# Performance work log

Measured on AMD Instinct MI355X. Metric: run time of the kernel, lower is better.

Reference implementation:

```python
import jax, jax.numpy as jnp
import numpy as np

LR = 0.01
EPS = 1e-8
D, H, O, N = 1024, 256, 64, 1024


def _normalize(W, b):
    # L2 (Frobenius) normalize weights and biases, clamped at EPS
    wn = jnp.maximum(jnp.sqrt(jnp.sum(W * W)), EPS)
    bn = jnp.maximum(jnp.sqrt(jnp.sum(b * b)), EPS)
    return W / wn, b / bn


def _step(carry, xt):
    W1, b1, W2, b2, W3, b3 = carry
    x, t = xt
    # forward pass (3-layer sigmoid MLP, softmax over -a3 as in original)
    a1 = jax.nn.sigmoid(x @ W1 + b1)
    a2 = jax.nn.sigmoid(a1 @ W2 + b2)
    a3 = jax.nn.sigmoid(a2 @ W3 + b3)
    out = jax.nn.softmax(-a3)
    # manual backprop deltas
    d3 = (t - out) * a3 * (1.0 - a3)
    o2 = (W3 @ d3) * a2 * (1.0 - a2)
    o1 = (W2 @ o2) * a1 * (1.0 - a1)
    # SGD update (note: original subtracts the delta, matching .sub_)
    W3 = W3 - LR * jnp.outer(a2, d3)
    b3 = b3 - LR * d3
    W2 = W2 - LR * jnp.outer(a1, o2)
    b2 = b2 - LR * o2
    W1 = W1 - LR * jnp.outer(x, o1)
    b1 = b1 - LR * o1
    # L2 normalize each layer's weights/biases
    W1, b1 = _normalize(W1, b1)
    W2, b2 = _normalize(W2, b2)
    W3, b3 = _normalize(W3, b3)
    return (W1, b1, W2, b2, W3, b3), None


def setup_inputs() -> dict:
    key = jax.random.key(0)
    k = jax.random.split(key, 5)
    return {
        "training_data": jax.random.normal(k[0], (N, D), jnp.float32),
        "training_targets": jax.random.uniform(k[1], (N, O), dtype=jnp.float32),
        "weights1": jax.random.normal(k[2], (D, H), jnp.float32) * 0.01,
        "biases1": jnp.zeros((H,), jnp.float32),
        "weights2": jax.random.normal(k[3], (H, H), jnp.float32) * 0.01,
        "biases2": jnp.zeros((H,), jnp.float32),
        "weights3": jax.random.normal(k[4], (H, O), jnp.float32) * 0.01,
        "biases3": jnp.zeros((O,), jnp.float32),
    }


def reference(training_data, training_targets, weights1, biases1, weights2, biases2, weights3, biases3):
    carry0 = (weights1, biases1, weights2, biases2, weights3, biases3)
    carry, _ = jax.lax.scan(_step, carry0, (training_data, training_targets))
    W1, b1, W2, b2, W3, b3 = carry
    return (W1, W2, W3)
```

## Files before the change

### kernel.cpp

```cpp
#include <hip/hip_runtime.h>
#include <math.h>


#define LRC  0.01f
#define EPSV 1e-8f

typedef float f32x8 __attribute__((ext_vector_type(8)));

#define SMEM_FLOATS 36368
#define SMEM_BYTES  (SMEM_FLOATS * 4)

#define ROWS16(OP)                                                            \
  OP(0) OP(1) OP(2) OP(3) OP(4) OP(5) OP(6) OP(7)                             \
  OP(8) OP(9) OP(10) OP(11) OP(12) OP(13) OP(14) OP(15)

__device__ __forceinline__ float hsum8(f32x8 v) {
  return ((v.s0 + v.s1) + (v.s2 + v.s3)) + ((v.s4 + v.s5) + (v.s6 + v.s7));
}

__device__ __forceinline__ float wave_allred(float v) {
#pragma unroll
  for (int off = 32; off > 0; off >>= 1) v += __shfl_xor(v, off);
  return v;
}

#define FMA16(c, a, b)                                                        \
  c[0][0] += a.x * b.x; c[0][1] += a.x * b.y; c[0][2] += a.x * b.z; c[0][3] += a.x * b.w; \
  c[1][0] += a.y * b.x; c[1][1] += a.y * b.y; c[1][2] += a.y * b.z; c[1][3] += a.y * b.w; \
  c[2][0] += a.z * b.x; c[2][1] += a.z * b.y; c[2][2] += a.z * b.z; c[2][3] += a.z * b.w; \
  c[3][0] += a.w * b.x; c[3][1] += a.w * b.y; c[3][2] += a.w * b.z; c[3][3] += a.w * b.w;

__global__ __launch_bounds__(256) void k_gram(const float* __restrict__ X,
                                              float* __restrict__ G) {
  const int bi = blockIdx.y, bj = blockIdx.x;
  if (bj > bi) return;
  __shared__ float Xa[32][68];
  __shared__ float Xb[32][68];
  const int tid = threadIdx.x;
  const int tx = tid & 15, ty = tid >> 4;
  float c[4][4] = {};
  for (int k0 = 0; k0 < 1024; k0 += 32) {
    __syncthreads();
    {
      const int row = tid >> 2, kk = (tid & 3) * 8;
      const float* pa = X + (bi * 64 + row) * 1024 + k0 + kk;
      const float4 a0 = *(const float4*)pa;
      const float4 a1 = *(const float4*)(pa + 4);
      Xa[kk + 0][row] = a0.x; Xa[kk + 1][row] = a0.y;
      Xa[kk + 2][row] = a0.z; Xa[kk + 3][row] = a0.w;
      Xa[kk + 4][row] = a1.x; Xa[kk + 5][row] = a1.y;
      Xa[kk + 6][row] = a1.z; Xa[kk + 7][row] = a1.w;
      const float* pb = X + (bj * 64 + row) * 1024 + k0 + kk;
      const float4 b0 = *(const float4*)pb;
      const float4 b1 = *(const float4*)(pb + 4);
      Xb[kk + 0][row] = b0.x; Xb[kk + 1][row] = b0.y;
      Xb[kk + 2][row] = b0.z; Xb[kk + 3][row] = b0.w;
      Xb[kk + 4][row] = b1.x; Xb[kk + 5][row] = b1.y;
      Xb[kk + 6][row] = b1.z; Xb[kk + 7][row] = b1.w;
    }
    __syncthreads();
#pragma unroll
    for (int kk = 0; kk < 32; kk++) {
      const float4 a = *(const float4*)&Xa[kk][ty * 4];
      const float4 b = *(const float4*)&Xb[kk][tx * 4];
      FMA16(c, a, b)
    }
  }
#pragma unroll
  for (int ii = 0; ii < 4; ii++) {
    *(float4*)(G + (bi * 64 + ty * 4 + ii) * 1024 + bj * 64 + tx * 4) =
        make_float4(c[ii][0], c[ii][1], c[ii][2], c[ii][3]);
  }
}

__global__ __launch_bounds__(256) void k_z10(const float* __restrict__ X,
                                             const float* __restrict__ W1g,
                                             float* __restrict__ Z10) {
  const int bi = blockIdx.y, bj = blockIdx.x;
  __shared__ float At[32][68];
  __shared__ float Bt[32][68];
  const int tid = threadIdx.x;
  const int tx = tid & 15, ty = tid >> 4;
  float c[4][4] = {};
  for (int k0 = 0; k0 < 1024; k0 += 32) {
    __syncthreads();
    {
      const int row = tid >> 2, kk = (tid & 3) * 8;
      const float* pa = X + (bi * 64 + row) * 1024 + k0 + kk;
      const float4 a0 = *(const float4*)pa;
      const float4 a1 = *(const float4*)(pa + 4);
      At[kk + 0][row] = a0.x; At[kk + 1][row] = a0.y;
      At[kk + 2][row] = a0.z; At[kk + 3][row] = a0.w;
      At[kk + 4][row] = a1.x; At[kk + 5][row] = a1.y;
      At[kk + 6][row] = a1.z; At[kk + 7][row] = a1.w;
      const int kr = tid >> 3, j8 = (tid & 7) * 8;
      const float* pb = W1g + (k0 + kr) * 256 + bj * 64 + j8;
      *(float4*)&Bt[kr][j8]     = *(const float4*)pb;
      *(float4*)&Bt[kr][j8 + 4] = *(const float4*)(pb + 4);
    }
    __syncthreads();
#pragma unroll
    for (int kk = 0; kk < 32; kk++) {
      const float4 a = *(const float4*)&At[kk][ty * 4];
      const float4 b = *(const float4*)&Bt[kk][tx * 4];
      FMA16(c, a, b)
    }
  }
#pragma unroll
  for (int ii = 0; ii < 4; ii++) {
    *(float4*)(Z10 + (bi * 64 + ty * 4 + ii) * 256 + bj * 64 + tx * 4) =
        make_float4(c[ii][0], c[ii][1], c[ii][2], c[ii][3]);
  }
}

__global__ __launch_bounds__(256) void k_w1out(
    const float* __restrict__ X, const float* __restrict__ o1g,
    const float* __restrict__ cg, const float* __restrict__ W1g,
    const float* __restrict__ sclg, float* __restrict__ outW1) {
  const int bi = blockIdx.y, bj = blockIdx.x;
  __shared__ float At[32][68];
  __shared__ float Bt[32][68];
  const int tid = threadIdx.x;
  const int tx = tid & 15, ty = tid >> 4;
  float c[4][4] = {};
  for (int k0 = 0; k0 < 1024; k0 += 32) {
    __syncthreads();
    {
      const int kr = tid >> 3, m8 = (tid & 7) * 8;
      const float* pa = X + (k0 + kr) * 1024 + bi * 64 + m8;
      *(float4*)&At[kr][m8]     = *(const float4*)pa;
      *(float4*)&At[kr][m8 + 4] = *(const float4*)(pa + 4);
      const float cs = cg[k0 + kr];
      const float* pb = o1g + (k0 + kr) * 256 + bj * 64 + m8;
      float4 b0 = *(const float4*)pb;
      float4 b1 = *(const float4*)(pb + 4);
      b0.x *= cs; b0.y *= cs; b0.z *= cs; b0.w *= cs;
      b1.x *= cs; b1.y *= cs; b1.z *= cs; b1.w *= cs;
      *(float4*)&Bt[kr][m8]     = b0;
      *(float4*)&Bt[kr][m8 + 4] = b1;
    }
    __syncthreads();
#pragma unroll
    for (int kk = 0; kk < 32; kk++) {
      const float4 a = *(const float4*)&At[kk][ty * 4];
      const float4 b = *(const float4*)&Bt[kk][tx * 4];
      FMA16(c, a, b)
    }
  }
  const float s1f = sclg[0];
#pragma unroll
  for (int ii = 0; ii < 4; ii++) {
    const int row = bi * 64 + ty * 4 + ii;
    const float4 w = *(const float4*)(W1g + row * 256 + bj * 64 + tx * 4);
    *(float4*)(outW1 + row * 256 + bj * 64 + tx * 4) =
        make_float4(s1f * (w.x + c[ii][0]), s1f * (w.y + c[ii][1]),
                    s1f * (w.z + c[ii][2]), s1f * (w.w + c[ii][3]));
  }
}

__device__ __forceinline__ float block_reduce8(float v, float* tmp, int tid) {
#pragma unroll
  for (int off = 32; off > 0; off >>= 1) v += __shfl_xor(v, off);
  __syncthreads();
  if ((tid & 63) == 0) tmp[tid >> 6] = v;
  __syncthreads();
  float s = 0.f;
#pragma unroll
  for (int w = 0; w < 8; w++) s += tmp[w];
  __syncthreads();
  return s;
}

__global__ __launch_bounds__(512, 1) void k2_seq(
    const float* __restrict__ Tg, const float* __restrict__ W1g,
    const float* __restrict__ b1g, const float* __restrict__ W2g,
    const float* __restrict__ b2g, const float* __restrict__ W3g,
    const float* __restrict__ b3g, const float* __restrict__ G,
    const float* __restrict__ Z10, float* __restrict__ o1g,
    float* __restrict__ cg, float* __restrict__ sclg,
    float* __restrict__ outW2, float* __restrict__ outW3) {
  extern __shared__ float sm[];
  float* const zo   = sm;
  float* const Gb   = sm + 17408;
  float* const scr  = sm + 21504;
  float* const Tb   = sm + 29952;
  float* const a1v  = sm + 34048;
  float* const z1v  = sm + 34560;
  float* const z2v  = sm + 34816;
  float* const a2v  = sm + 35072;
  float* const o2v  = sm + 35328;
  float* const b1ps = sm + 35584;
  float* const b2ps = sm + 35840;
  float* const d3v  = sm + 36096;
  float* const b3ps = sm + 36160;
  float* const ch   = sm + 36224;
  float* const dpart= sm + 36288;
  float* const sca  = sm + 36328;
  float* const cpre = sm + 36336;

  const int tid = threadIdx.x;
  const int p = tid >> 5;
  const int q = tid & 31;

  f32x8 W2_0, W2_1, W2_2, W2_3, W2_4, W2_5, W2_6, W2_7,
        W2_8, W2_9, W2_10, W2_11, W2_12, W2_13, W2_14, W2_15;
  float W3x_0, W3x_1, W3x_2, W3x_3, W3x_4, W3x_5, W3x_6, W3x_7,
        W3x_8, W3x_9, W3x_10, W3x_11, W3x_12, W3x_13, W3x_14, W3x_15;
  float W3y_0, W3y_1, W3y_2, W3y_3, W3y_4, W3y_5, W3y_6, W3y_7,
        W3y_8, W3y_9, W3y_10, W3y_11, W3y_12, W3y_13, W3y_14, W3y_15;

#define INIT_ROW(i)                                                           \
  { const int row = p * 16 + i;                                               \
    W2_##i  = *(const f32x8*)(W2g + row * 256 + q * 8);                       \
    W3x_##i = W3g[row * 64 + q * 2];                                          \
    W3y_##i = W3g[row * 64 + q * 2 + 1]; }
  ROWS16(INIT_ROW)

  if (tid < 256) { b1ps[tid] = b1g[tid]; b2ps[tid] = b2g[tid]; }
  if (tid < 64) b3ps[tid] = b3g[tid];
  if (tid == 0) {
    sca[0] = 1.f; sca[1] = 1.f; sca[2] = 1.f; sca[3] = 1.f;
    sca[4] = 1.f; sca[5] = 1.f; sca[6] = 0.f; sca[7] = 0.f;
  }

  float acc1 = 0.f;
  for (int i = tid; i < 65536; i += 512) {
    const float4 v = ((const float4*)W1g)[i];
    acc1 += v.x * v.x + v.y * v.y + v.z * v.z + v.w * v.w;
  }
  const float n1init = block_reduce8(acc1, scr, tid);
  float acc2 = 0.f;
#define N2_ROW(i) { f32x8 t = W2_##i * W2_##i; acc2 += hsum8(t); }
  ROWS16(N2_ROW)
  const float n2init = block_reduce8(acc2, scr, tid);
  float acc3 = 0.f;
#define N3_ROW(i) acc3 += W3x_##i * W3x_##i + W3y_##i * W3y_##i;
  ROWS16(N3_ROW)
  const float n3init = block_reduce8(acc3, scr, tid);

  float s1 = 1.f, s2 = 1.f, s3 = 1.f;
  double n1d = (double)n1init;
  float n2 = n2init, n3 = n3init;
  __syncthreads();

  for (int b = 0; b < 16; b++) {
    const int bs = b * 64;
    {
      f32x8 pacc0 = {0.f, 0.f, 0.f, 0.f, 0.f, 0.f, 0.f, 0.f};
      f32x8 pacc1 = pacc0, pacc2 = pacc0, pacc3 = pacc0;
      for (int c0 = 0; c0 < bs; c0 += 32) {
        __syncthreads();
        if (tid < 32) cpre[tid] = cg[c0 + tid];
        {
          const int row = tid >> 3, k4 = (tid & 7) * 4;
          const float4 gv = *(const float4*)(G + (bs + row) * 1024 + c0 + k4);
          Gb[row * 33 + k4 + 0] = gv.x; Gb[row * 33 + k4 + 1] = gv.y;
          Gb[row * 33 + k4 + 2] = gv.z; Gb[row * 33 + k4 + 3] = gv.w;
        }
#pragma unroll
        for (int u = 0; u < 4; u++) {
          const int fi = tid + u * 512;
          ((float4*)scr)[fi] = ((const float4*)(o1g + c0 * 256))[fi];
        }
        __syncthreads();
#pragma unroll 2
        for (int ss = 0; ss < 32; ss++) {
          const float cs = cpre[ss];
          const f32x8 o8 = *(const f32x8*)(scr + ss * 256 + q * 8);
          pacc0 += (Gb[(p * 4 + 0) * 33 + ss] * cs) * o8;
          pacc1 += (Gb[(p * 4 + 1) * 33 + ss] * cs) * o8;
          pacc2 += (Gb[(p * 4 + 2) * 33 + ss] * cs) * o8;
          pacc3 += (Gb[(p * 4 + 3) * 33 + ss] * cs) * o8;
        }
      }
      __syncthreads();
#define ZSTORE(rr)                                                            \
      { const int row = p * 4 + rr;                                           \
        *(f32x8*)(zo + row * 272 + q * 8) =                                   \
            *(const f32x8*)(Z10 + (bs + row) * 256 + q * 8) + pacc##rr; }
      ZSTORE(0) ZSTORE(1) ZSTORE(2) ZSTORE(3)
#pragma unroll
      for (int u = 0; u < 2; u++) {
        const int fi = tid + u * 512;
        const int row = fi >> 4, c4 = fi & 15;
        *(float4*)(Gb + row * 64 + c4 * 4) =
            *(const float4*)(G + (bs + row) * 1024 + bs + c4 * 4);
      }
      ((float4*)Tb)[tid]       = ((const float4*)(Tg + bs * 64))[tid];
      ((float4*)Tb)[tid + 512] = ((const float4*)(Tg + bs * 64))[tid + 512];
      __syncthreads();
    }

    for (int l = 0; l < 64; l++) {
      const int t = bs + l;
      const int cur = (t & 1) * 256, prv = 256 - cur;
      const float s1c = sca[0], rb1c = sca[1], s2c = sca[2],
                  rb2c = sca[3], s3c = sca[4], rb3c = sca[5];
      if (t > 0) {
        const float cw2 = sca[6], cw3 = sca[7];
        const f32x8 o8s = cw2 * (*(const f32x8*)&o2v[q * 8]);
        const float d0s = cw3 * d3v[q * 2], d1s = cw3 * d3v[q * 2 + 1];
#define UPD_ROW(i)                                                            \
        { const float a1o = a1v[prv + p * 16 + i];                            \
          W2_##i += a1o * o8s;                                                \
          const float a2o = a2v[p * 16 + i];                                  \
          W3x_##i += a2o * d0s; W3y_##i += a2o * d1s; }
        ROWS16(UPD_ROW)
      }
      {
        const int j = tid >> 1, half = tid & 1;
        float a = 0.f;
        for (int lp = half; lp < l; lp += 2)
          a += ch[lp] * Gb[l * 64 + lp] * zo[lp * 272 + j];
        a += __shfl_xor(a, 1);
        if (half == 0) {
          const float z1u = zo[l * 272 + j] + a;
          z1v[j] = z1u;
          const float z = s1c * z1u + rb1c * b1ps[j];
          a1v[cur + j] = 1.f / (1.f + expf(-z));
        }
      }
      __syncthreads();
      {
        f32x8 acc = {0.f, 0.f, 0.f, 0.f, 0.f, 0.f, 0.f, 0.f};
#define B1_ROW(i) acc += a1v[cur + p * 16 + i] * W2_##i;
        ROWS16(B1_ROW)
        *(f32x8*)&scr[p * 264 + q * 8] = acc;
      }
      __syncthreads();
      if (tid < 256) {
        float s = 0.f;
#pragma unroll
        for (int pp = 0; pp < 16; pp++) s += scr[pp * 264 + tid];
        const float z2p = s2c * s;
        z2v[tid] = z2p;
        a2v[tid] = 1.f / (1.f + expf(-(z2p + rb2c * b2ps[tid])));
      }
      __syncthreads();
      {
        float c0a = 0.f, c1a = 0.f;
#define C1_ROW(i)                                                             \
        { const float a2x = a2v[p * 16 + i];                                  \
          c0a += a2x * W3x_##i; c1a += a2x * W3y_##i; }
        ROWS16(C1_ROW)
        scr[(q * 2 + 0) * 17 + p] = c0a;
        scr[(q * 2 + 1) * 17 + p] = c1a;
      }
      __syncthreads();
      if (tid < 64) {
        float s = 0.f;
#pragma unroll
        for (int pp = 0; pp < 16; pp++) s += scr[tid * 17 + pp];
        const float z3p = s3c * s;
        const float a3 = 1.f / (1.f + expf(-(z3p + rb3c * b3ps[tid])));
        const float e = expf(-a3);
        const float tot = wave_allred(e);
        const float outv = e / tot;
        const float d3 = (Tb[l * 64 + tid] - outv) * a3 * (1.f - a3);
        d3v[tid] = d3;
        const float b3n = rb3c * b3ps[tid] - LRC * d3;
        b3ps[tid] = b3n;
        const float v5 = wave_allred(z3p * d3);
        const float v7 = wave_allred(d3 * d3);
        const float v10 = wave_allred(b3n * b3n);
        if (tid == 0) { dpart[32] = v5; dpart[33] = v7; dpart[34] = v10; }
      }
      __syncthreads();
      {
        const float d0 = d3v[q * 2 + 0], d1 = d3v[q * 2 + 1];
#define E1_ROW(i) scr[(p * 16 + i) * 33 + q] = W3x_##i * d0 + W3y_##i * d1;
        ROWS16(E1_ROW)
      }
      __syncthreads();
      if (tid < 256) {
        float s = 0.f;
#pragma unroll
        for (int qq = 0; qq < 32; qq++) s += scr[tid * 33 + qq];
        const float a2x = a2v[tid];
        const float o2 = s3c * s * a2x * (1.f - a2x);
        o2v[tid] = o2;
        const float b2n = rb2c * b2ps[tid] - LRC * o2;
        b2ps[tid] = b2n;
        const float v2 = wave_allred(z2v[tid] * o2);
        const float v4 = wave_allred(o2 * o2);
        const float v6 = wave_allred(a2x * a2x);
        const float v9 = wave_allred(b2n * b2n);
        if ((tid & 63) == 0) {
          const int w = tid >> 6;
          dpart[16 + w] = v2; dpart[20 + w] = v4;
          dpart[24 + w] = v6; dpart[28 + w] = v9;
        }
      }
      __syncthreads();
      {
        const f32x8 ov8 = *(const f32x8*)&o2v[q * 8];
#define F1_ROW(i)                                                             \
        { f32x8 tmp = W2_##i * ov8; scr[(p * 16 + i) * 33 + q] = hsum8(tmp); }
        ROWS16(F1_ROW)
      }
      __syncthreads();
      if (tid < 256) {
        float s = 0.f;
#pragma unroll
        for (int qq = 0; qq < 32; qq++) s += scr[tid * 33 + qq];
        const float a1x = a1v[cur + tid];
        const float o1x = s2c * s * a1x * (1.f - a1x);
        zo[l * 272 + tid] = o1x;
        const float b1n = rb1c * b1ps[tid] - LRC * o1x;
        b1ps[tid] = b1n;
        const float v0 = wave_allred(z1v[tid] * o1x);
        const float v1 = wave_allred(o1x * o1x);
        const float v3 = wave_allred(a1x * a1x);
        const float v8 = wave_allred(b1n * b1n);
        if ((tid & 63) == 0) {
          const int w = tid >> 6;
          dpart[0 + w] = v0; dpart[4 + w] = v1;
          dpart[8 + w] = v3; dpart[12 + w] = v8;
        }
      }
      __syncthreads();
      if (tid < 64) {
        const float dts0 = (dpart[0] + dpart[1]) + (dpart[2] + dpart[3]);
        const float dts1 = (dpart[4] + dpart[5]) + (dpart[6] + dpart[7]);
        const float dts3 = (dpart[8] + dpart[9]) + (dpart[10] + dpart[11]);
        const float dts8 = (dpart[12] + dpart[13]) + (dpart[14] + dpart[15]);
        const float dts2 = (dpart[16] + dpart[17]) + (dpart[18] + dpart[19]);
        const float dts4 = (dpart[20] + dpart[21]) + (dpart[22] + dpart[23]);
        const float dts6 = (dpart[24] + dpart[25]) + (dpart[26] + dpart[27]);
        const float dts9 = (dpart[28] + dpart[29]) + (dpart[30] + dpart[31]);
        const float dts5 = dpart[32], dts7 = dpart[33], dts10 = dpart[34];
        const float c1 = -LRC / s1;
        const double gtt = (double)Gb[l * 64 + l];
        n1d = n1d + 2.0 * (double)c1 * (double)dts0 +
              (double)c1 * (double)c1 * gtt * (double)dts1;
        const double w1n = (double)s1 * sqrt(n1d);
        s1 = (float)((double)s1 / fmax(w1n, (double)EPSV));
        const float n2p = n2 - 2.f * LRC * dts2 + LRC * LRC * dts3 * dts4;
        const float r2s = 1.f / fmaxf(sqrtf(n2p), EPSV);
        n2 = n2p * r2s * r2s;
        const float cw2 = -LRC / s2;
        s2 = s2 * r2s;
        const float n3p = n3 - 2.f * LRC * dts5 + LRC * LRC * dts6 * dts7;
        const float r3s = 1.f / fmaxf(sqrtf(n3p), EPSV);
        n3 = n3p * r3s * r3s;
        const float cw3 = -LRC / s3;
        s3 = s3 * r3s;
        if (tid == 0) {
          ch[l] = c1;
          sca[0] = s1;
          sca[1] = 1.f / fmaxf(sqrtf(dts8), EPSV);
          sca[2] = s2;
          sca[3] = 1.f / fmaxf(sqrtf(dts9), EPSV);
          sca[4] = s3;
          sca[5] = 1.f / fmaxf(sqrtf(dts10), EPSV);
          sca[6] = cw2;
          sca[7] = cw3;
        }
      }
      __syncthreads();
    }

    {
#pragma unroll
      for (int u = 0; u < 4; u++) {
        const int chunk = tid + u * 512;
        const int row = chunk >> 5, c8 = chunk & 31;
        *(f32x8*)(o1g + (bs + row) * 256 + c8 * 8) =
            *(const f32x8*)(zo + row * 272 + c8 * 8);
      }
      if (tid < 64) cg[bs + tid] = ch[tid];
    }
  }

  {
    const float cw2 = sca[6], cw3 = sca[7];
    const float s2f = sca[2], s3f = sca[4];
    const f32x8 o8s = cw2 * (*(const f32x8*)&o2v[q * 8]);
    const float d0s = cw3 * d3v[q * 2], d1s = cw3 * d3v[q * 2 + 1];
#define FIN_ROW(i)                                                            \
    { const float a1o = a1v[256 + p * 16 + i];          \
      W2_##i += a1o * o8s;                                                    \
      const float a2o = a2v[p * 16 + i];                                      \
      W3x_##i += a2o * d0s; W3y_##i += a2o * d1s;                             \
      const int row = p * 16 + i;                                             \
      *(f32x8*)(outW2 + row * 256 + q * 8) = s2f * W2_##i;                    \
      outW3[row * 64 + q * 2]     = s3f * W3x_##i;                            \
      outW3[row * 64 + q * 2 + 1] = s3f * W3y_##i; }
    ROWS16(FIN_ROW)
    if (tid == 0) sclg[0] = sca[0];
  }
}

extern "C" void kernel_launch(void* const* d_in, const int* in_sizes, int n_in,
                              void* d_out, int out_size, void* d_ws,
                              size_t ws_size, hipStream_t stream) {
  (void)in_sizes; (void)n_in; (void)out_size; (void)ws_size;
  const float* X   = (const float*)d_in[0];
  const float* Tg  = (const float*)d_in[1];
  const float* W1g = (const float*)d_in[2];
  const float* b1g = (const float*)d_in[3];
  const float* W2g = (const float*)d_in[4];
  const float* b2g = (const float*)d_in[5];
  const float* W3g = (const float*)d_in[6];
  const float* b3g = (const float*)d_in[7];
  float* out = (float*)d_out;
  float* ws  = (float*)d_ws;

  float* G    = ws;
  float* Z10  = G + 1048576;
  float* o1g  = Z10 + 262144;
  float* cg   = o1g + 262144;
  float* sclg = cg + 1024;

  (void)hipFuncSetAttribute((const void*)k2_seq,
                            hipFuncAttributeMaxDynamicSharedMemorySize,
                            SMEM_BYTES);

  k_gram<<<dim3(16, 16), 256, 0, stream>>>(X, G);
  k_z10<<<dim3(4, 16), 256, 0, stream>>>(X, W1g, Z10);
  k2_seq<<<dim3(1), dim3(512), SMEM_BYTES, stream>>>(
      Tg, W1g, b1g, W2g, b2g, W3g, b3g, G, Z10, o1g, cg, sclg,
      out + 262144, out + 327680);
  k_w1out<<<dim3(4, 16), 256, 0, stream>>>(X, o1g, cg, W1g, sclg, out);
}
```

Measured before the change: 10.22 ms.

## Remap W2/W3 register tiles per wave to cut block barriers per step

Changes how the register-resident W2 and W3 are partitioned: each wave now owns a 32-column slab of W2 (4 rows per lane) and a 32x64 slab of W3. Matrix-vector products are reduced inside the wave with a shuffle transpose-reduce tree instead of through shared-memory scratch plus extra __syncthreads. The goal is to shrink the number of block-wide barriers and serialized tid<256 reduction phases in the sequential per-sample loop from about eight to four. The cost is redundant per-wave work, wave-local LDS fences, double-buffered b3, and a more complex ordering of the norm partial sums.

```diff
diff --git a/kernel.cpp b/kernel.cpp
--- a/kernel.cpp
+++ b/kernel.cpp
@@ -7,12 +7,8 @@
 
 typedef float f32x8 __attribute__((ext_vector_type(8)));
 
-#define SMEM_FLOATS 36368
+#define SMEM_FLOATS 36696
 #define SMEM_BYTES  (SMEM_FLOATS * 4)
-
-#define ROWS16(OP)                                                            \
-  OP(0) OP(1) OP(2) OP(3) OP(4) OP(5) OP(6) OP(7)                             \
-  OP(8) OP(9) OP(10) OP(11) OP(12) OP(13) OP(14) OP(15)
 
 __device__ __forceinline__ float hsum8(f32x8 v) {
   return ((v.s0 + v.s1) + (v.s2 + v.s3)) + ((v.s4 + v.s5) + (v.s6 + v.s7));
@@ -22,6 +18,30 @@
 #pragma unroll
   for (int off = 32; off > 0; off >>= 1) v += __shfl_xor(v, off);
   return v;
+}
+
+__device__ __forceinline__ void wave_fence() {
+  __builtin_amdgcn_sched_barrier(0);
+  asm volatile("s_waitcnt lgkmcnt(0)" ::: "memory");
+  __builtin_amdgcn_sched_barrier(0);
+}
+
+__device__ __forceinline__ float xtree32(float v[32], const int lane) {
+#pragma unroll
+  for (int m = 1; m <= 16; m <<= 1) {
+    const int n2 = 16 / m;
+    const bool hi = (lane & m) != 0;
+#pragma unroll
+    for (int s = 0; s < n2; s++) {
+      const float a = v[2 * s], b = v[2 * s + 1];
+      const float send = hi ? a : b;
+      const float keep = hi ? b : a;
+      v[s] = keep + __shfl_xor(send, m);
+    }
+  }
+  float r = v[0];
+  r += __shfl_xor(r, 32);
+  return r;
 }
 
 #define FMA16(c, a, b)                                                        \
@@ -171,6 +191,12 @@
   return s;
 }
 
+#define JK_LIST(OP) OP(0,0,0) OP(0,1,1) OP(0,2,2) OP(0,3,3)                   \
+                    OP(1,0,4) OP(1,1,5) OP(1,2,6) OP(1,3,7)                   \
+                    OP(2,0,8) OP(2,1,9) OP(2,2,10) OP(2,3,11)                 \
+                    OP(3,0,12) OP(3,1,13) OP(3,2,14) OP(3,3,15)
+#define K_LIST(OP) OP(0) OP(1) OP(2) OP(3)
+
 __global__ __launch_bounds__(512, 1) void k2_seq(
     const float* __restrict__ Tg, const float* __restrict__ W1g,
     const float* __restrict__ b1g, const float* __restrict__ W2g,
@@ -180,41 +206,45 @@
     float* __restrict__ cg, float* __restrict__ sclg,
     float* __restrict__ outW2, float* __restrict__ outW3) {
   extern __shared__ float sm[];
-  float* const zo   = sm;
-  float* const Gb   = sm + 17408;
-  float* const scr  = sm + 21504;
-  float* const Tb   = sm + 29952;
-  float* const a1v  = sm + 34048;
-  float* const z1v  = sm + 34560;
-  float* const z2v  = sm + 34816;
-  float* const a2v  = sm + 35072;
-  float* const o2v  = sm + 35328;
-  float* const b1ps = sm + 35584;
-  float* const b2ps = sm + 35840;
-  float* const d3v  = sm + 36096;
-  float* const b3ps = sm + 36160;
-  float* const ch   = sm + 36224;
-  float* const dpart= sm + 36288;
-  float* const sca  = sm + 36328;
-  float* const cpre = sm + 36336;
+  float* const zo    = sm;
+  float* const Gb    = sm + 17408;
+  float* const scr   = sm + 21504;
+  float* const Tb    = sm + 29952;
+  float* const a1v   = sm + 34048;
+  float* const zk    = sm + 34560;
+  float* const a2v   = sm + 34816;
+  float* const o2v   = sm + 35072;
+  float* const b1ps  = sm + 35328;
+  float* const b2ps  = sm + 35584;
+  float* const zp    = sm + 35840;
+  float* const d3v   = sm + 36352;
+  float* const b3ps  = sm + 36416;
+  float* const ch    = sm + 36544;
+  float* const dpart = sm + 36608;
+  float* const sca   = sm + 36656;
+  float* const cpre  = sm + 36664;
 
   const int tid = threadIdx.x;
-  const int p = tid >> 5;
-  const int q = tid & 31;
+  const int lane = tid & 63;
+  const int w = tid >> 6;
+  const int p = tid >> 5, q = tid & 31;
+  const int rbase = 4 * lane;
+  const int cbase = 32 * w;
 
   f32x8 W2_0, W2_1, W2_2, W2_3, W2_4, W2_5, W2_6, W2_7,
         W2_8, W2_9, W2_10, W2_11, W2_12, W2_13, W2_14, W2_15;
-  float W3x_0, W3x_1, W3x_2, W3x_3, W3x_4, W3x_5, W3x_6, W3x_7,
-        W3x_8, W3x_9, W3x_10, W3x_11, W3x_12, W3x_13, W3x_14, W3x_15;
-  float W3y_0, W3y_1, W3y_2, W3y_3, W3y_4, W3y_5, W3y_6, W3y_7,
-        W3y_8, W3y_9, W3y_10, W3y_11, W3y_12, W3y_13, W3y_14, W3y_15;
-
-#define INIT_ROW(i)                                                           \
-  { const int row = p * 16 + i;                                               \
-    W2_##i  = *(const f32x8*)(W2g + row * 256 + q * 8);                       \
-    W3x_##i = W3g[row * 64 + q * 2];                                          \
-    W3y_##i = W3g[row * 64 + q * 2 + 1]; }
-  ROWS16(INIT_ROW)
+  f32x8 W3v8_0, W3v8_1, W3v8_2, W3v8_3;
+
+#define INIT_W2(j, k, idx)                                                    \
+  W2_##idx = *(const f32x8*)(W2g + (rbase + j) * 256 + cbase + 8 * k);
+  JK_LIST(INIT_W2)
+
+#define INIT_W3(k)                                                            \
+  { const float* p3 = W3g + (cbase + 8 * k) * 64 + lane;                      \
+    W3v8_##k[0] = p3[0];   W3v8_##k[1] = p3[64];  W3v8_##k[2] = p3[128];      \
+    W3v8_##k[3] = p3[192]; W3v8_##k[4] = p3[256]; W3v8_##k[5] = p3[320];      \
+    W3v8_##k[6] = p3[384]; W3v8_##k[7] = p3[448]; }
+  K_LIST(INIT_W3)
 
   if (tid < 256) { b1ps[tid] = b1g[tid]; b2ps[tid] = b2g[tid]; }
   if (tid < 64) b3ps[tid] = b3g[tid];
@@ -230,12 +260,12 @@
   }
   const float n1init = block_reduce8(acc1, scr, tid);
   float acc2 = 0.f;
-#define N2_ROW(i) { f32x8 t = W2_##i * W2_##i; acc2 += hsum8(t); }
-  ROWS16(N2_ROW)
+#define N2R(j, k, idx) { f32x8 tq = W2_##idx * W2_##idx; acc2 += hsum8(tq); }
+  JK_LIST(N2R)
   const float n2init = block_reduce8(acc2, scr, tid);
   float acc3 = 0.f;
-#define N3_ROW(i) acc3 += W3x_##i * W3x_##i + W3y_##i * W3y_##i;
-  ROWS16(N3_ROW)
+#define N3R(k) { f32x8 tq = W3v8_##k * W3v8_##k; acc3 += hsum8(tq); }
+  K_LIST(N3R)
   const float n3init = block_reduce8(acc3, scr, tid);
 
   float s1 = 1.f, s2 = 1.f, s3 = 1.f;
@@ -294,18 +324,30 @@
     for (int l = 0; l < 64; l++) {
       const int t = bs + l;
       const int cur = (t & 1) * 256, prv = 256 - cur;
+      const int pb = (t & 1) * 64;
       const float s1c = sca[0], rb1c = sca[1], s2c = sca[2],
                   rb2c = sca[3], s3c = sca[4], rb3c = sca[5];
+
       if (t > 0) {
         const float cw2 = sca[6], cw3 = sca[7];
-        const f32x8 o8s = cw2 * (*(const f32x8*)&o2v[q * 8]);
-        const float d0s = cw3 * d3v[q * 2], d1s = cw3 * d3v[q * 2 + 1];
-#define UPD_ROW(i)                                                            \
-        { const float a1o = a1v[prv + p * 16 + i];                            \
-          W2_##i += a1o * o8s;                                                \
-          const float a2o = a2v[p * 16 + i];                                  \
-          W3x_##i += a2o * d0s; W3y_##i += a2o * d1s; }
-        ROWS16(UPD_ROW)
+        const f32x8 oc0 = cw2 * (*(const f32x8*)&o2v[cbase]);
+        const f32x8 oc1 = cw2 * (*(const f32x8*)&o2v[cbase + 8]);
+        const f32x8 oc2 = cw2 * (*(const f32x8*)&o2v[cbase + 16]);
+        const f32x8 oc3 = cw2 * (*(const f32x8*)&o2v[cbase + 24]);
+        const float4 a1o = *(const float4*)&a1v[prv + rbase];
+        W2_0  += a1o.x * oc0; W2_1  += a1o.x * oc1;
+        W2_2  += a1o.x * oc2; W2_3  += a1o.x * oc3;
+        W2_4  += a1o.y * oc0; W2_5  += a1o.y * oc1;
+        W2_6  += a1o.y * oc2; W2_7  += a1o.y * oc3;
+        W2_8  += a1o.z * oc0; W2_9  += a1o.z * oc1;
+        W2_10 += a1o.z * oc2; W2_11 += a1o.z * oc3;
+        W2_12 += a1o.w * oc0; W2_13 += a1o.w * oc1;
+        W2_14 += a1o.w * oc2; W2_15 += a1o.w * oc3;
+        const float d3s = cw3 * d3v[lane];
+        W3v8_0 += d3s * (*(const f32x8*)&a2v[cbase]);
+        W3v8_1 += d3s * (*(const f32x8*)&a2v[cbase + 8]);
+        W3v8_2 += d3s * (*(const f32x8*)&a2v[cbase + 16]);
+        W3v8_3 += d3s * (*(const f32x8*)&a2v[cbase + 24]);
       }
       {
         const int j = tid >> 1, half = tid & 1;
@@ -313,122 +355,136 @@
         for (int lp = half; lp < l; lp += 2)
           a += ch[lp] * Gb[l * 64 + lp] * zo[lp * 272 + j];
         a += __shfl_xor(a, 1);
+        float a1x = 0.f;
         if (half == 0) {
           const float z1u = zo[l * 272 + j] + a;
-          z1v[j] = z1u;
           const float z = s1c * z1u + rb1c * b1ps[j];
-          a1v[cur + j] = 1.f / (1.f + expf(-z));
-        }
+          a1x = 1.f / (1.f + expf(-z));
+          a1v[cur + j] = a1x;
+          zk[j] = z1u * a1x * (1.f - a1x);
+        }
+        const float v3 = wave_allred(a1x * a1x);
+        if (lane == 0) dpart[w] = v3;
       }
       __syncthreads();
+
+      float z2p, a2own;
       {
-        f32x8 acc = {0.f, 0.f, 0.f, 0.f, 0.f, 0.f, 0.f, 0.f};
-#define B1_ROW(i) acc += a1v[cur + p * 16 + i] * W2_##i;
-        ROWS16(B1_ROW)
-        *(f32x8*)&scr[p * 264 + q * 8] = acc;
+        const float4 a1q = *(const float4*)&a1v[cur + rbase];
+        const f32x8 vz0 = a1q.x * W2_0 + a1q.y * W2_4 + a1q.z * W2_8  + a1q.w * W2_12;
+        const f32x8 vz1 = a1q.x * W2_1 + a1q.y * W2_5 + a1q.z * W2_9  + a1q.w * W2_13;
+        const f32x8 vz2 = a1q.x * W2_2 + a1q.y * W2_6 + a1q.z * W2_10 + a1q.w * W2_14;
+        const f32x8 vz3 = a1q.x * W2_3 + a1q.y * W2_7 + a1q.z * W2_11 + a1q.w * W2_15;
+        alignas(32) float v[32];
+        *(f32x8*)&v[0] = vz0;  *(f32x8*)&v[8] = vz1;
+        *(f32x8*)&v[16] = vz2; *(f32x8*)&v[24] = vz3;
+        const float z2sum = xtree32(v, lane);
+        const int c = cbase + (lane & 31);
+        z2p = s2c * z2sum;
+        a2own = 1.f / (1.f + expf(-(z2p + rb2c * b2ps[c])));
+        if (lane < 32) a2v[c] = a2own;
+        wave_fence();
+        const f32x8 a2b0 = *(const f32x8*)&a2v[cbase];
+        const f32x8 a2b1 = *(const f32x8*)&a2v[cbase + 8];
+        const f32x8 a2b2 = *(const f32x8*)&a2v[cbase + 16];
+        const f32x8 a2b3 = *(const f32x8*)&a2v[cbase + 24];
+        const f32x8 zacc = a2b0 * W3v8_0 + a2b1 * W3v8_1 +
+                           a2b2 * W3v8_2 + a2b3 * W3v8_3;
+        zp[w * 64 + lane] = hsum8(zacc);
+        const float v6 = wave_allred(a2own * a2own);
+        if (lane == 0) dpart[8 + w] = v6;
       }
       __syncthreads();
-      if (tid < 256) {
-        float s = 0.f;
-#pragma unroll
-        for (int pp = 0; pp < 16; pp++) s += scr[pp * 264 + tid];
-        const float z2p = s2c * s;
-        z2v[tid] = z2p;
-        a2v[tid] = 1.f / (1.f + expf(-(z2p + rb2c * b2ps[tid])));
-      }
-      __syncthreads();
+
+      float dts5 = 0.f, dts7 = 0.f, dts10 = 0.f;
       {
-        float c0a = 0.f, c1a = 0.f;
-#define C1_ROW(i)                                                             \
-        { const float a2x = a2v[p * 16 + i];                                  \
-          c0a += a2x * W3x_##i; c1a += a2x * W3y_##i; }
-        ROWS16(C1_ROW)
-        scr[(q * 2 + 0) * 17 + p] = c0a;
-        scr[(q * 2 + 1) * 17 + p] = c1a;
-      }
-      __syncthreads();
-      if (tid < 64) {
-        float s = 0.f;
-#pragma unroll
-        for (int pp = 0; pp < 16; pp++) s += scr[tid * 17 + pp];
-        const float z3p = s3c * s;
-        const float a3 = 1.f / (1.f + expf(-(z3p + rb3c * b3ps[tid])));
+        float z3s = 0.f;
+#pragma unroll
+        for (int w2 = 0; w2 < 8; w2++) z3s += zp[w2 * 64 + lane];
+        const float z3p = s3c * z3s;
+        const float a3 = 1.f / (1.f + expf(-(z3p + rb3c * b3ps[pb + lane])));
         const float e = expf(-a3);
         const float tot = wave_allred(e);
         const float outv = e / tot;
-        const float d3 = (Tb[l * 64 + tid] - outv) * a3 * (1.f - a3);
-        d3v[tid] = d3;
-        const float b3n = rb3c * b3ps[tid] - LRC * d3;
-        b3ps[tid] = b3n;
-        const float v5 = wave_allred(z3p * d3);
-        const float v7 = wave_allred(d3 * d3);
-        const float v10 = wave_allred(b3n * b3n);
-        if (tid == 0) { dpart[32] = v5; dpart[33] = v7; dpart[34] = v10; }
+        const float d3 = (Tb[l * 64 + lane] - outv) * a3 * (1.f - a3);
+        if (w == 0) {
+          const float b3n = rb3c * b3ps[pb + lane] - LRC * d3;
+          b3ps[(64 - pb) + lane] = b3n;
+          d3v[lane] = d3;
+          dts5 = wave_allred(z3p * d3);
+          dts7 = wave_allred(d3 * d3);
+          dts10 = wave_allred(b3n * b3n);
+        }
+        alignas(32) float v[32];
+        *(f32x8*)&v[0]  = W3v8_0 * d3;
+        *(f32x8*)&v[8]  = W3v8_1 * d3;
+        *(f32x8*)&v[16] = W3v8_2 * d3;
+        *(f32x8*)&v[24] = W3v8_3 * d3;
+        const float o2raw = xtree32(v, lane);
+        const int r = cbase + (lane & 31);
+        const float o2x = s3c * o2raw * a2own * (1.f - a2own);
+        const float b2o = b2ps[r];
+        const float b2n = rb2c * b2o - LRC * o2x;
+        if (lane < 32) { b2ps[r] = b2n; o2v[r] = o2x; }
+        wave_fence();
+        const f32x8 ob0 = *(const f32x8*)&o2v[cbase];
+        const f32x8 ob1 = *(const f32x8*)&o2v[cbase + 8];
+        const f32x8 ob2 = *(const f32x8*)&o2v[cbase + 16];
+        const f32x8 ob3 = *(const f32x8*)&o2v[cbase + 24];
+        const f32x8 fa0 = W2_0 * ob0 + W2_1 * ob1 + W2_2 * ob2 + W2_3 * ob3;
+        const f32x8 fa1 = W2_4 * ob0 + W2_5 * ob1 + W2_6 * ob2 + W2_7 * ob3;
+        const f32x8 fa2 = W2_8 * ob0 + W2_9 * ob1 + W2_10 * ob2 + W2_11 * ob3;
+        const f32x8 fa3 = W2_12 * ob0 + W2_13 * ob1 + W2_14 * ob2 + W2_15 * ob3;
+        const float f0 = hsum8(fa0), f1 = hsum8(fa1),
+                    f2 = hsum8(fa2), f3 = hsum8(fa3);
+        *(float4*)&scr[w * 256 + rbase] = make_float4(f0, f1, f2, f3);
+        const float4 zkq = *(const float4*)&zk[rbase];
+        const float v0 = wave_allred(zkq.x * f0 + zkq.y * f1 +
+                                     zkq.z * f2 + zkq.w * f3);
+        const float v2 = wave_allred(z2p * o2x);
+        const float v4 = wave_allred(o2x * o2x);
+        const float v9 = wave_allred(b2n * b2n);
+        if (lane == 0) {
+          dpart[16 + w] = v0; dpart[24 + w] = v2;
+          dpart[32 + w] = v4; dpart[40 + w] = v9;
+        }
       }
       __syncthreads();
-      {
-        const float d0 = d3v[q * 2 + 0], d1 = d3v[q * 2 + 1];
-#define E1_ROW(i) scr[(p * 16 + i) * 33 + q] = W3x_##i * d0 + W3y_##i * d1;
-        ROWS16(E1_ROW)
-      }
-      __syncthreads();
-      if (tid < 256) {
-        float s = 0.f;
-#pragma unroll
-        for (int qq = 0; qq < 32; qq++) s += scr[tid * 33 + qq];
-        const float a2x = a2v[tid];
-        const float o2 = s3c * s * a2x * (1.f - a2x);
-        o2v[tid] = o2;
-        const float b2n = rb2c * b2ps[tid] - LRC * o2;
-        b2ps[tid] = b2n;
-        const float v2 = wave_allred(z2v[tid] * o2);
-        const float v4 = wave_allred(o2 * o2);
-        const float v6 = wave_allred(a2x * a2x);
-        const float v9 = wave_allred(b2n * b2n);
-        if ((tid & 63) == 0) {
-          const int w = tid >> 6;
-          dpart[16 + w] = v2; dpart[20 + w] = v4;
-          dpart[24 + w] = v6; dpart[28 + w] = v9;
-        }
-      }
-      __syncthreads();
-      {
-        const f32x8 ov8 = *(const f32x8*)&o2v[q * 8];
-#define F1_ROW(i)                                                             \
-        { f32x8 tmp = W2_##i * ov8; scr[(p * 16 + i) * 33 + q] = hsum8(tmp); }
-        ROWS16(F1_ROW)
-      }
-      __syncthreads();
-      if (tid < 256) {
-        float s = 0.f;
-#pragma unroll
-        for (int qq = 0; qq < 32; qq++) s += scr[tid * 33 + qq];
-        const float a1x = a1v[cur + tid];
-        const float o1x = s2c * s * a1x * (1.f - a1x);
-        zo[l * 272 + tid] = o1x;
-        const float b1n = rb1c * b1ps[tid] - LRC * o1x;
-        b1ps[tid] = b1n;
-        const float v0 = wave_allred(z1v[tid] * o1x);
-        const float v1 = wave_allred(o1x * o1x);
-        const float v3 = wave_allred(a1x * a1x);
-        const float v8 = wave_allred(b1n * b1n);
-        if ((tid & 63) == 0) {
-          const int w = tid >> 6;
-          dpart[0 + w] = v0; dpart[4 + w] = v1;
-          dpart[8 + w] = v3; dpart[12 + w] = v8;
-        }
-      }
-      __syncthreads();
-      if (tid < 64) {
-        const float dts0 = (dpart[0] + dpart[1]) + (dpart[2] + dpart[3]);
-        const float dts1 = (dpart[4] + dpart[5]) + (dpart[6] + dpart[7]);
-        const float dts3 = (dpart[8] + dpart[9]) + (dpart[10] + dpart[11]);
-        const float dts8 = (dpart[12] + dpart[13]) + (dpart[14] + dpart[15]);
-        const float dts2 = (dpart[16] + dpart[17]) + (dpart[18] + dpart[19]);
-        const float dts4 = (dpart[20] + dpart[21]) + (dpart[22] + dpart[23]);
-        const float dts6 = (dpart[24] + dpart[25]) + (dpart[26] + dpart[27]);
-        const float dts9 = (dpart[28] + dpart[29]) + (dpart[30] + dpart[31]);
-        const float dts5 = dpart[32], dts7 = dpart[33], dts10 = dpart[34];
+
+      if (w == 0) {
+        float4 s4 = make_float4(0.f, 0.f, 0.f, 0.f);
+#pragma unroll
+        for (int w2 = 0; w2 < 8; w2++) {
+          const float4 pv = *(const float4*)&scr[w2 * 256 + rbase];
+          s4.x += pv.x; s4.y += pv.y; s4.z += pv.z; s4.w += pv.w;
+        }
+        const float4 a1q = *(const float4*)&a1v[cur + rbase];
+        const float o1a = s2c * s4.x * a1q.x * (1.f - a1q.x);
+        const float o1b = s2c * s4.y * a1q.y * (1.f - a1q.y);
+        const float o1c = s2c * s4.z * a1q.z * (1.f - a1q.z);
+        const float o1d = s2c * s4.w * a1q.w * (1.f - a1q.w);
+        *(float4*)&zo[l * 272 + rbase] = make_float4(o1a, o1b, o1c, o1d);
+        const float4 b1q = *(const float4*)&b1ps[rbase];
+        const float b1a = rb1c * b1q.x - LRC * o1a;
+        const float b1b = rb1c * b1q.y - LRC * o1b;
+        const float b1cc = rb1c * b1q.z - LRC * o1c;
+        const float b1d = rb1c * b1q.w - LRC * o1d;
+        *(float4*)&b1ps[rbase] = make_float4(b1a, b1b, b1cc, b1d);
+        const float dts1 = wave_allred(o1a * o1a + o1b * o1b +
+                                       o1c * o1c + o1d * o1d);
+        const float dts8 = wave_allred(b1a * b1a + b1b * b1b +
+                                       b1cc * b1cc + b1d * b1d);
+        float dts3 = 0.f, dts6h = 0.f, dts0r = 0.f,
+              dts2h = 0.f, dts4h = 0.f, dts9h = 0.f;
+#pragma unroll
+        for (int u = 0; u < 8; u++) {
+          dts3  += dpart[u];      dts6h += dpart[8 + u];
+          dts0r += dpart[16 + u]; dts2h += dpart[24 + u];
+          dts4h += dpart[32 + u]; dts9h += dpart[40 + u];
+        }
+        const float dts0 = s2c * dts0r;
+        const float dts2 = 0.5f * dts2h, dts4 = 0.5f * dts4h,
+                    dts6 = 0.5f * dts6h, dts9 = 0.5f * dts9h;
         const float c1 = -LRC / s1;
         const double gtt = (double)Gb[l * 64 + l];
         n1d = n1d + 2.0 * (double)c1 * (double)dts0 +
@@ -438,14 +494,14 @@
         const float n2p = n2 - 2.f * LRC * dts2 + LRC * LRC * dts3 * dts4;
         const float r2s = 1.f / fmaxf(sqrtf(n2p), EPSV);
         n2 = n2p * r2s * r2s;
-        const float cw2 = -LRC / s2;
+        const float cw2n = -LRC / s2;
         s2 = s2 * r2s;
         const float n3p = n3 - 2.f * LRC * dts5 + LRC * LRC * dts6 * dts7;
         const float r3s = 1.f / fmaxf(sqrtf(n3p), EPSV);
         n3 = n3p * r3s * r3s;
-        const float cw3 = -LRC / s3;
+        const float cw3n = -LRC / s3;
         s3 = s3 * r3s;
-        if (tid == 0) {
+        if (lane == 0) {
           ch[l] = c1;
           sca[0] = s1;
           sca[1] = 1.f / fmaxf(sqrtf(dts8), EPSV);
@@ -453,8 +509,8 @@
           sca[3] = 1.f / fmaxf(sqrtf(dts9), EPSV);
           sca[4] = s3;
           sca[5] = 1.f / fmaxf(sqrtf(dts10), EPSV);
-          sca[6] = cw2;
-          sca[7] = cw3;
+          sca[6] = cw2n;
+          sca[7] = cw3n;
         }
       }
       __syncthreads();
@@ -475,18 +531,35 @@
   {
     const float cw2 = sca[6], cw3 = sca[7];
     const float s2f = sca[2], s3f = sca[4];
-    const f32x8 o8s = cw2 * (*(const f32x8*)&o2v[q * 8]);
-    const float d0s = cw3 * d3v[q * 2], d1s = cw3 * d3v[q * 2 + 1];
-#define FIN_ROW(i)                                                            \
-    { const float a1o = a1v[256 + p * 16 + i];          \
-      W2_##i += a1o * o8s;                                                    \
-      const float a2o = a2v[p * 16 + i];                                      \
-      W3x_##i += a2o * d0s; W3y_##i += a2o * d1s;                             \
-      const int row = p * 16 + i;                                             \
-      *(f32x8*)(outW2 + row * 256 + q * 8) = s2f * W2_##i;                    \
-      outW3[row * 64 + q * 2]     = s3f * W3x_##i;                            \
-      outW3[row * 64 + q * 2 + 1] = s3f * W3y_##i; }
-    ROWS16(FIN_ROW)
+    const f32x8 oc0 = cw2 * (*(const f32x8*)&o2v[cbase]);
+    const f32x8 oc1 = cw2 * (*(const f32x8*)&o2v[cbase + 8]);
+    const f32x8 oc2 = cw2 * (*(const f32x8*)&o2v[cbase + 16]);
+    const f32x8 oc3 = cw2 * (*(const f32x8*)&o2v[cbase + 24]);
+    const float4 a1o = *(const float4*)&a1v[256 + rbase];
+    W2_0  += a1o.x * oc0; W2_1  += a1o.x * oc1;
+    W2_2  += a1o.x * oc2; W2_3  += a1o.x * oc3;
+    W2_4  += a1o.y * oc0; W2_5  += a1o.y * oc1;
+    W2_6  += a1o.y * oc2; W2_7  += a1o.y * oc3;
+    W2_8  += a1o.z * oc0; W2_9  += a1o.z * oc1;
+    W2_10 += a1o.z * oc2; W2_11 += a1o.z * oc3;
+    W2_12 += a1o.w * oc0; W2_13 += a1o.w * oc1;
+    W2_14 += a1o.w * oc2; W2_15 += a1o.w * oc3;
+    const float d3s = cw3 * d3v[lane];
+    W3v8_0 += d3s * (*(const f32x8*)&a2v[cbase]);
+    W3v8_1 += d3s * (*(const f32x8*)&a2v[cbase + 8]);
+    W3v8_2 += d3s * (*(const f32x8*)&a2v[cbase + 16]);
+    W3v8_3 += d3s * (*(const f32x8*)&a2v[cbase + 24]);
+
+#define OUT_W2(j, k, idx)                                                     \
+    *(f32x8*)(outW2 + (rbase + j) * 256 + cbase + 8 * k) = s2f * W2_##idx;
+    JK_LIST(OUT_W2)
+#define OUT_W3(k)                                                             \
+    { float* p3 = outW3 + (cbase + 8 * k) * 64 + lane;                        \
+      p3[0]   = s3f * W3v8_##k[0]; p3[64]  = s3f * W3v8_##k[1];               \
+      p3[128] = s3f * W3v8_##k[2]; p3[192] = s3f * W3v8_##k[3];               \
+      p3[256] = s3f * W3v8_##k[4]; p3[320] = s3f * W3v8_##k[5];               \
+      p3[384] = s3f * W3v8_##k[6]; p3[448] = s3f * W3v8_##k[7]; }
+    K_LIST(OUT_W3)
     if (tid == 0) sclg[0] = sca[0];
   }
 }
```

Result: slower. 10.92 ms (+6.9%).

## Use DPP wave reductions and move layer-2/3 norm updates off the serial tail

Applied to the files above, without the earlier changes.

Replaces the shuffle-based wave all-reduce with DPP row/bcast adds plus a readlane, which avoids the LDS traffic of ds_swizzle/bpermute-style shuffles on the critical per-timestep path. Reworks the z1 recurrence so four lanes each produce two outputs, with float2 loads and a DPP quad reduction, and computes the a1 squared-norm there. The layer-2/3 normalization scalars are now computed by wave 7 during the F1 phase instead of in the final single-wave serial block, which shortens that block. Shared-memory layout is adjusted to hold the extra partials. This adds reliance on DPP control encodings being correct for wave64.

```diff
diff --git a/kernel.cpp b/kernel.cpp
--- a/kernel.cpp
+++ b/kernel.cpp
@@ -7,7 +7,7 @@
 
 typedef float f32x8 __attribute__((ext_vector_type(8)));
 
-#define SMEM_FLOATS 36368
+#define SMEM_FLOATS 36384
 #define SMEM_BYTES  (SMEM_FLOATS * 4)
 
 #define ROWS16(OP)                                                            \
@@ -16,6 +16,24 @@
 
 __device__ __forceinline__ float hsum8(f32x8 v) {
   return ((v.s0 + v.s1) + (v.s2 + v.s3)) + ((v.s4 + v.s5) + (v.s6 + v.s7));
+}
+
+template <int CTRL>
+__device__ __forceinline__ float dpp_add(float v) {
+  const int s = __builtin_amdgcn_update_dpp(0, __builtin_bit_cast(int, v),
+                                            CTRL, 0xf, 0xf, true);
+  return v + __builtin_bit_cast(float, s);
+}
+
+__device__ __forceinline__ float dpp_allred64(float v) {
+  v = dpp_add<0x111>(v);
+  v = dpp_add<0x112>(v);
+  v = dpp_add<0x114>(v);
+  v = dpp_add<0x118>(v);
+  v = dpp_add<0x142>(v);
+  v = dpp_add<0x143>(v);
+  return __builtin_bit_cast(float,
+      __builtin_amdgcn_readlane(__builtin_bit_cast(int, v), 63));
 }
 
 __device__ __forceinline__ float wave_allred(float v) {
@@ -159,8 +177,7 @@
 }
 
 __device__ __forceinline__ float block_reduce8(float v, float* tmp, int tid) {
-#pragma unroll
-  for (int off = 32; off > 0; off >>= 1) v += __shfl_xor(v, off);
+  v = wave_allred(v);
   __syncthreads();
   if ((tid & 63) == 0) tmp[tid >> 6] = v;
   __syncthreads();
@@ -195,10 +212,12 @@
   float* const b3ps = sm + 36160;
   float* const ch   = sm + 36224;
   float* const dpart= sm + 36288;
-  float* const sca  = sm + 36328;
-  float* const cpre = sm + 36336;
+  float* const sca  = sm + 36336;
+  float* const cpre = sm + 36352;
 
   const int tid = threadIdx.x;
+  const int lane = tid & 63;
+  const int w = tid >> 6;
   const int p = tid >> 5;
   const int q = tid & 31;
 
@@ -296,6 +315,7 @@
       const int cur = (t & 1) * 256, prv = 256 - cur;
       const float s1c = sca[0], rb1c = sca[1], s2c = sca[2],
                   rb2c = sca[3], s3c = sca[4], rb3c = sca[5];
+
       if (t > 0) {
         const float cw2 = sca[6], cw3 = sca[7];
         const f32x8 o8s = cw2 * (*(const f32x8*)&o2v[q * 8]);
@@ -308,17 +328,27 @@
         ROWS16(UPD_ROW)
       }
       {
-        const int j = tid >> 1, half = tid & 1;
-        float a = 0.f;
-        for (int lp = half; lp < l; lp += 2)
-          a += ch[lp] * Gb[l * 64 + lp] * zo[lp * 272 + j];
-        a += __shfl_xor(a, 1);
-        if (half == 0) {
-          const float z1u = zo[l * 272 + j] + a;
-          z1v[j] = z1u;
-          const float z = s1c * z1u + rb1c * b1ps[j];
-          a1v[cur + j] = 1.f / (1.f + expf(-z));
-        }
+        const int jp = tid >> 2, quarter = tid & 3;
+        float ax = 0.f, ay = 0.f;
+        for (int lp = quarter; lp < l; lp += 4) {
+          const float gcs = ch[lp] * Gb[l * 64 + lp];
+          const float2 zr = *(const float2*)&zo[lp * 272 + 2 * jp];
+          ax += gcs * zr.x; ay += gcs * zr.y;
+        }
+        ax = dpp_add<0xB1>(ax); ax = dpp_add<0x4E>(ax);
+        ay = dpp_add<0xB1>(ay); ay = dpp_add<0x4E>(ay);
+        const float2 zop = *(const float2*)&zo[l * 272 + 2 * jp];
+        const float2 b1q = *(const float2*)&b1ps[2 * jp];
+        const float z1u0 = zop.x + ax, z1u1 = zop.y + ay;
+        const float a1x0 = 1.f / (1.f + expf(-(s1c * z1u0 + rb1c * b1q.x)));
+        const float a1x1 = 1.f / (1.f + expf(-(s1c * z1u1 + rb1c * b1q.y)));
+        if (quarter == 0) {
+          *(float2*)&z1v[2 * jp] = make_float2(z1u0, z1u1);
+          *(float2*)&a1v[cur + 2 * jp] = make_float2(a1x0, a1x1);
+        }
+        const float v3 = dpp_allred64(
+            quarter == 0 ? a1x0 * a1x0 + a1x1 * a1x1 : 0.f);
+        if (lane == 0) dpart[36 + w] = v3;
       }
       __syncthreads();
       {
@@ -354,15 +384,15 @@
         const float z3p = s3c * s;
         const float a3 = 1.f / (1.f + expf(-(z3p + rb3c * b3ps[tid])));
         const float e = expf(-a3);
-        const float tot = wave_allred(e);
+        const float tot = dpp_allred64(e);
         const float outv = e / tot;
         const float d3 = (Tb[l * 64 + tid] - outv) * a3 * (1.f - a3);
         d3v[tid] = d3;
         const float b3n = rb3c * b3ps[tid] - LRC * d3;
         b3ps[tid] = b3n;
-        const float v5 = wave_allred(z3p * d3);
-        const float v7 = wave_allred(d3 * d3);
-        const float v10 = wave_allred(b3n * b3n);
+        const float v5 = dpp_allred64(z3p * d3);
+        const float v7 = dpp_allred64(d3 * d3);
+        const float v10 = dpp_allred64(b3n * b3n);
         if (tid == 0) { dpart[32] = v5; dpart[33] = v7; dpart[34] = v10; }
       }
       __syncthreads();
@@ -381,12 +411,11 @@
         o2v[tid] = o2;
         const float b2n = rb2c * b2ps[tid] - LRC * o2;
         b2ps[tid] = b2n;
-        const float v2 = wave_allred(z2v[tid] * o2);
-        const float v4 = wave_allred(o2 * o2);
-        const float v6 = wave_allred(a2x * a2x);
-        const float v9 = wave_allred(b2n * b2n);
+        const float v2 = dpp_allred64(z2v[tid] * o2);
+        const float v4 = dpp_allred64(o2 * o2);
+        const float v6 = dpp_allred64(a2x * a2x);
+        const float v9 = dpp_allred64(b2n * b2n);
         if ((tid & 63) == 0) {
-          const int w = tid >> 6;
           dpart[16 + w] = v2; dpart[20 + w] = v4;
           dpart[24 + w] = v6; dpart[28 + w] = v9;
         }
@@ -397,6 +426,33 @@
 #define F1_ROW(i)                                                             \
         { f32x8 tmp = W2_##i * ov8; scr[(p * 16 + i) * 33 + q] = hsum8(tmp); }
         ROWS16(F1_ROW)
+      }
+      if (w == 7) {
+        const float dts3 = ((dpart[36] + dpart[37]) + (dpart[38] + dpart[39]))
+                         + ((dpart[40] + dpart[41]) + (dpart[42] + dpart[43]));
+        const float dts2 = (dpart[16] + dpart[17]) + (dpart[18] + dpart[19]);
+        const float dts4 = (dpart[20] + dpart[21]) + (dpart[22] + dpart[23]);
+        const float dts6 = (dpart[24] + dpart[25]) + (dpart[26] + dpart[27]);
+        const float dts9 = (dpart[28] + dpart[29]) + (dpart[30] + dpart[31]);
+        const float dts5 = dpart[32], dts7 = dpart[33], dts10 = dpart[34];
+        const float n2p = n2 - 2.f * LRC * dts2 + LRC * LRC * dts3 * dts4;
+        const float r2s = 1.f / fmaxf(sqrtf(n2p), EPSV);
+        n2 = n2p * r2s * r2s;
+        const float cw2n = -LRC / s2;
+        s2 = s2 * r2s;
+        const float n3p = n3 - 2.f * LRC * dts5 + LRC * LRC * dts6 * dts7;
+        const float r3s = 1.f / fmaxf(sqrtf(n3p), EPSV);
+        n3 = n3p * r3s * r3s;
+        const float cw3n = -LRC / s3;
+        s3 = s3 * r3s;
+        if (lane == 0) {
+          sca[2] = s2;
+          sca[3] = 1.f / fmaxf(sqrtf(dts9), EPSV);
+          sca[4] = s3;
+          sca[5] = 1.f / fmaxf(sqrtf(dts10), EPSV);
+          sca[6] = cw2n;
+          sca[7] = cw3n;
+        }
       }
       __syncthreads();
       if (tid < 256) {
@@ -408,53 +464,28 @@
         zo[l * 272 + tid] = o1x;
         const float b1n = rb1c * b1ps[tid] - LRC * o1x;
         b1ps[tid] = b1n;
-        const float v0 = wave_allred(z1v[tid] * o1x);
-        const float v1 = wave_allred(o1x * o1x);
-        const float v3 = wave_allred(a1x * a1x);
-        const float v8 = wave_allred(b1n * b1n);
+        const float v0 = dpp_allred64(z1v[tid] * o1x);
+        const float v1 = dpp_allred64(o1x * o1x);
+        const float v8 = dpp_allred64(b1n * b1n);
         if ((tid & 63) == 0) {
-          const int w = tid >> 6;
-          dpart[0 + w] = v0; dpart[4 + w] = v1;
-          dpart[8 + w] = v3; dpart[12 + w] = v8;
+          dpart[0 + w] = v0; dpart[4 + w] = v1; dpart[12 + w] = v8;
         }
       }
       __syncthreads();
       if (tid < 64) {
         const float dts0 = (dpart[0] + dpart[1]) + (dpart[2] + dpart[3]);
         const float dts1 = (dpart[4] + dpart[5]) + (dpart[6] + dpart[7]);
-        const float dts3 = (dpart[8] + dpart[9]) + (dpart[10] + dpart[11]);
         const float dts8 = (dpart[12] + dpart[13]) + (dpart[14] + dpart[15]);
-        const float dts2 = (dpart[16] + dpart[17]) + (dpart[18] + dpart[19]);
-        const float dts4 = (dpart[20] + dpart[21]) + (dpart[22] + dpart[23]);
-        const float dts6 = (dpart[24] + dpart[25]) + (dpart[26] + dpart[27]);
-        const float dts9 = (dpart[28] + dpart[29]) + (dpart[30] + dpart[31]);
-        const float dts5 = dpart[32], dts7 = dpart[33], dts10 = dpart[34];
         const float c1 = -LRC / s1;
         const double gtt = (double)Gb[l * 64 + l];
         n1d = n1d + 2.0 * (double)c1 * (double)dts0 +
               (double)c1 * (double)c1 * gtt * (double)dts1;
         const double w1n = (double)s1 * sqrt(n1d);
         s1 = (float)((double)s1 / fmax(w1n, (double)EPSV));
-        const float n2p = n2 - 2.f * LRC * dts2 + LRC * LRC * dts3 * dts4;
-        const float r2s = 1.f / fmaxf(sqrtf(n2p), EPSV);
-        n2 = n2p * r2s * r2s;
-        const float cw2 = -LRC / s2;
-        s2 = s2 * r2s;
-        const float n3p = n3 - 2.f * LRC * dts5 + LRC * LRC * dts6 * dts7;
-        const float r3s = 1.f / fmaxf(sqrtf(n3p), EPSV);
-        n3 = n3p * r3s * r3s;
-        const float cw3 = -LRC / s3;
-        s3 = s3 * r3s;
         if (tid == 0) {
           ch[l] = c1;
           sca[0] = s1;
           sca[1] = 1.f / fmaxf(sqrtf(dts8), EPSV);
-          sca[2] = s2;
-          sca[3] = 1.f / fmaxf(sqrtf(dts9), EPSV);
-          sca[4] = s3;
-          sca[5] = 1.f / fmaxf(sqrtf(dts10), EPSV);
-          sca[6] = cw2;
-          sca[7] = cw3;
         }
       }
       __syncthreads();
```

After: 8.963 ms. -12.3%, faster.
